# Optimization experiments

Measured on AMD Instinct MI355X. Metric: run time of the kernel, lower is better.

## Reference

```python
import jax, jax.numpy as jnp
import numpy as np

B, T, C = 4, 2048, 2048
H = 16
D = C // H  # head_dim = 128
THETA = 10000.0


def rope_cos_sin(t, d, dtype=jnp.float32):
    inv_freq = 1.0 / (THETA ** (jnp.arange(0, d, 2, dtype=jnp.float32) / d))  # [D/2]
    pos = jnp.arange(t, dtype=jnp.float32)
    freqs = jnp.outer(pos, inv_freq)                 # [T, D/2]
    emb = jnp.concatenate([freqs, freqs], axis=-1)   # [T, D]
    return jnp.cos(emb).astype(dtype), jnp.sin(emb).astype(dtype)


def rotate_half(x):
    x1, x2 = jnp.split(x, 2, axis=-1)
    return jnp.concatenate([-x2, x1], axis=-1)


def setup_inputs() -> dict:
    key = jax.random.key(0)
    k1, k2, k3 = jax.random.split(key, 3)
    x = jax.random.normal(k1, (B, T, C), dtype=jnp.float32)
    Wqkv = jax.random.normal(k2, (C, 3 * C), dtype=jnp.float32) * (1.0 / np.sqrt(C))
    Wout = jax.random.normal(k3, (C, C), dtype=jnp.float32) * (1.0 / np.sqrt(C))
    return {"x": x, "Wqkv": Wqkv, "Wout": Wout}


def reference(x, Wqkv, Wout):
    b, t, c = x.shape
    qkv = jnp.einsum('btc,cd->btd', x, Wqkv)          # [B,T,3C]
    q, k, v = jnp.split(qkv, 3, axis=-1)
    # [B,T,C] -> [B,H,T,D]
    q = q.reshape(b, t, H, D).transpose(0, 2, 1, 3)
    k = k.reshape(b, t, H, D).transpose(0, 2, 1, 3)
    v = v.reshape(b, t, H, D).transpose(0, 2, 1, 3)
    cos, sin = rope_cos_sin(t, D, x.dtype)            # [T,D]
    cos = cos[None, None]                             # [1,1,T,D]
    sin = sin[None, None]
    q = q * cos + rotate_half(q) * sin
    k = k * cos + rotate_half(k) * sin
    scale = 1.0 / np.sqrt(D)
    scores = jnp.einsum('bhqd,bhkd->bhqk', q, k) * scale
    causal = jnp.tril(jnp.ones((t, t), dtype=bool))
    scores = jnp.where(causal[None, None], scores, jnp.finfo(scores.dtype).min)
    attn = jax.nn.softmax(scores, axis=-1)
    y = jnp.einsum('bhqk,bhkd->bhqd', attn, v)        # [B,H,T,D]
    y = y.transpose(0, 2, 1, 3).reshape(b, t, c)      # [B,T,C]
    return jnp.einsum('btc,cd->btd', y, Wout)
```

## Files before the change

### kernel.cpp

```cpp
#include <hip/hip_runtime.h>
#include <hip/hip_bf16.h>
#include <cmath>

#define Bsz   4
#define Tlen  2048
#define Cdim  2048
#define Hn    16
#define Dh    128
#define N_QKV 6144
#define Mrows 8192

typedef __bf16 bf16x8 __attribute__((ext_vector_type(8)));
typedef __bf16 bf16x4 __attribute__((ext_vector_type(4)));
typedef float  f32x4  __attribute__((ext_vector_type(4)));
typedef uint32_t u32x2 __attribute__((ext_vector_type(2)));

__device__ __forceinline__ f32x4 mfma16(bf16x8 a, bf16x8 b, f32x4 c) {
  return __builtin_amdgcn_mfma_f32_16x16x32_bf16(a, b, c, 0, 0, 0);
}

__device__ __forceinline__ void gl16(const void* g, void* l) {
  __builtin_amdgcn_global_load_lds(
      (const __attribute__((address_space(1))) void*)g,
      (__attribute__((address_space(3))) void*)l, 16, 0, 0);
}

__device__ __forceinline__ uint32_t pack_bf16(float lo, float hi) {
  union { __bf16 h; unsigned short u; } a, b;
  a.h = (__bf16)lo; b.h = (__bf16)hi;
  return (uint32_t)a.u | ((uint32_t)b.u << 16);
}

__global__ void rope_table_k(float* __restrict__ cosT, float* __restrict__ sinT) {
  int idx = blockIdx.x * 256 + threadIdx.x;
  int t = idx >> 6, i = idx & 63;
  float invf = __expf(-(float)i * 0.14391156698f);
  float a = (float)t * invf;
  float s, c;
  sincosf(a, &s, &c);
  cosT[idx] = c;
  sinT[idx] = s;
}

__global__ __launch_bounds__(256) void f32_to_bf16_k(
    const float* __restrict__ src, __bf16* __restrict__ dst) {
  size_t i = ((size_t)blockIdx.x * 256 + threadIdx.x) * 8;
  f32x4 a = *(const f32x4*)(src + i);
  f32x4 b = *(const f32x4*)(src + i + 4);
  bf16x8 o;
  o[0] = (__bf16)a[0]; o[1] = (__bf16)a[1]; o[2] = (__bf16)a[2]; o[3] = (__bf16)a[3];
  o[4] = (__bf16)b[0]; o[5] = (__bf16)b[1]; o[6] = (__bf16)b[2]; o[7] = (__bf16)b[3];
  *(bf16x8*)(dst + i) = o;
}

__global__ __launch_bounds__(256) void transpose_to_bf16_k(
    const float* __restrict__ src, __bf16* __restrict__ dst, int K, int N) {
  __shared__ float tile[32][33];
  int n0 = blockIdx.x * 32, k0 = blockIdx.y * 32;
  int tr = threadIdx.x >> 3, tc = (threadIdx.x & 7) * 4;
  f32x4 v = *(const f32x4*)&src[(size_t)(k0 + tr) * N + n0 + tc];
  tile[tr][tc + 0] = v[0]; tile[tr][tc + 1] = v[1];
  tile[tr][tc + 2] = v[2]; tile[tr][tc + 3] = v[3];
  __syncthreads();
  bf16x4 w;
  w[0] = (__bf16)tile[tc + 0][tr];
  w[1] = (__bf16)tile[tc + 1][tr];
  w[2] = (__bf16)tile[tc + 2][tr];
  w[3] = (__bf16)tile[tc + 3][tr];
  *(bf16x4*)&dst[(size_t)(n0 + tr) * K + k0 + tc] = w;
}

__global__ __launch_bounds__(512, 2) void qkv_gemm(
    const __bf16* __restrict__ Xb, const __bf16* __restrict__ Wt,
    __bf16* __restrict__ Qo, __bf16* __restrict__ Ko, __bf16* __restrict__ Vo,
    const float* __restrict__ cosT, const float* __restrict__ sinT)
{
  __shared__ union SM {
    struct { __bf16 A[2][256 * 64]; __bf16 B[2][256 * 64]; } s;
    float C[64][265];
  } sm;

  const int tid = threadIdx.x, lane = tid & 63, wid = tid >> 6;
  const int g = lane >> 4, l16 = lane & 15;
  const int wr = wid >> 2, wc = wid & 3;

  const int bid = blockIdx.x;
  const int xcd = bid & 7, idx = bid >> 3;
  const int stl = idx >> 4, pos = idx & 15;
  const int m0 = (xcd * 4 + (pos >> 2)) * 256;
  const int n0 = (stl * 4 + (pos & 3)) * 256;

  const int srow = tid >> 3;
  const int schk = (tid & 7) ^ (srow & 7);
  const __bf16* gA = Xb + (size_t)(m0 + srow) * Cdim + schk * 8;
  const __bf16* gB = Wt + (size_t)(n0 + srow) * Cdim + schk * 8;
  const int ldst = wid * 512;

  f32x4 acc[8][4] = {};
  const int NT = Cdim / 64;

  #pragma unroll
  for (int r = 0; r < 4; ++r) {
    gl16(gA + (size_t)r * 64 * Cdim, &sm.s.A[0][r * 4096 + ldst]);
    gl16(gB + (size_t)r * 64 * Cdim, &sm.s.B[0][r * 4096 + ldst]);
  }
  #pragma unroll
  for (int r = 0; r < 4; ++r) {
    gl16(gA + 64 + (size_t)r * 64 * Cdim, &sm.s.A[1][r * 4096 + ldst]);
    gl16(gB + 64 + (size_t)r * 64 * Cdim, &sm.s.B[1][r * 4096 + ldst]);
  }

  for (int t = 0; t < NT; ++t) {
    const int p = t & 1;
    if (t < NT - 1) asm volatile("s_waitcnt vmcnt(8)" ::: "memory");
    else            asm volatile("s_waitcnt vmcnt(0)" ::: "memory");
    __builtin_amdgcn_s_barrier();
    __builtin_amdgcn_sched_barrier(0);

    #pragma unroll
    for (int kk = 0; kk < 2; ++kk) {
      bf16x8 a[8], b[4];
      const int ch = (((kk << 2) | g) ^ (l16 & 7)) * 8;
      #pragma unroll
      for (int f = 0; f < 8; ++f)
        a[f] = *(const bf16x8*)&sm.s.A[p][(wr * 128 + f * 16 + l16) * 64 + ch];
      #pragma unroll
      for (int n = 0; n < 4; ++n)
        b[n] = *(const bf16x8*)&sm.s.B[p][(wc * 64 + n * 16 + l16) * 64 + ch];
      #pragma unroll
      for (int f = 0; f < 8; ++f)
        #pragma unroll
        for (int n = 0; n < 4; ++n)
          acc[f][n] = mfma16(a[f], b[n], acc[f][n]);
    }

    __builtin_amdgcn_sched_barrier(0);
    asm volatile("s_waitcnt lgkmcnt(0)" ::: "memory");
    __builtin_amdgcn_s_barrier();

    if (t + 2 < NT) {
      const __bf16* pA = gA + (size_t)(t + 2) * 64;
      const __bf16* pB = gB + (size_t)(t + 2) * 64;
      #pragma unroll
      for (int r = 0; r < 4; ++r) {
        gl16(pA + (size_t)r * 64 * Cdim, &sm.s.A[p][r * 4096 + ldst]);
        gl16(pB + (size_t)r * 64 * Cdim, &sm.s.B[p][r * 4096 + ldst]);
      }
    }
  }

  const int sel = n0 >> 11;
  const int h0  = (n0 & 2047) >> 7;
  const int erow = tid >> 3, q = tid & 7;
  const int dlo = (q & 3) * 16;
  const int clo = (q >> 2) * 128 + dlo;
  const int vcol = tid >> 1, vth = tid & 1;

  #pragma unroll
  for (int rh = 0; rh < 4; ++rh) {
    if (wr == (rh >> 1)) {
      const int fb = (rh & 1) * 4;
      #pragma unroll
      for (int f2 = 0; f2 < 4; ++f2)
        #pragma unroll
        for (int n = 0; n < 4; ++n)
          #pragma unroll
          for (int r = 0; r < 4; ++r)
            sm.C[f2 * 16 + g * 4 + r][wc * 64 + n * 16 + l16] = acc[fb + f2][n][r];
    }
    __syncthreads();
    if (sel == 2) {
      const int hh = h0 + (vcol >> 7), d = vcol & 127;
      const int mb = m0 + rh * 64 + vth * 32;
      const int b_ = mb >> 11, tt = mb & 2047;
      __bf16* outp = Vo + (((size_t)(b_ * Hn + hh)) * Dh + d) * Tlen + tt;
      bf16x8 w[4];
      #pragma unroll
      for (int i = 0; i < 32; ++i)
        w[i >> 3][i & 7] = (__bf16)sm.C[vth * 32 + i][vcol];
      #pragma unroll
      for (int k = 0; k < 4; ++k) *(bf16x8*)&outp[k * 8] = w[k];
    } else {
      __bf16* dst = (sel == 0) ? Qo : Ko;
      const int m = m0 + rh * 64 + erow;
      const int b_ = m >> 11, t = m & 2047;
      __bf16* out = dst + (((size_t)(b_ * Hn + h0 + (q >> 2))) * Tlen + t) * Dh + dlo;
      const float* cb = cosT + t * 64 + dlo;
      const float* sb = sinT + t * 64 + dlo;
      bf16x8 o1[2], o2[2];
      #pragma unroll
      for (int i = 0; i < 16; ++i) {
        float v1 = sm.C[erow][clo + i];
        float v2 = sm.C[erow][clo + i + 64];
        float cs = cb[i], sn = sb[i];
        float r1 = v1 * cs - v2 * sn;
        float r2 = v2 * cs + v1 * sn;
        o1[i >> 3][i & 7] = (__bf16)r1;
        o2[i >> 3][i & 7] = (__bf16)r2;
      }
      *(bf16x8*)&out[0]  = o1[0];
      *(bf16x8*)&out[8]  = o1[1];
      *(bf16x8*)&out[64] = o2[0];
      *(bf16x8*)&out[72] = o2[1];
    }
    __syncthreads();
  }
}

__global__ __launch_bounds__(256, 2) void attn_fwd(
    const __bf16* __restrict__ Qg, const __bf16* __restrict__ Kg,
    const __bf16* __restrict__ Vtg, __bf16* __restrict__ Yg)
{
  __shared__ __bf16 Ks[2][64 * 128];
  __shared__ __bf16 Vt[2][128 * 64];
  __shared__ uint32_t Ps2[4][16 * 34 + 2];

  const int tid = threadIdx.x, lane = tid & 63, wid = tid >> 6;
  const int g = lane >> 4, l16 = lane & 15;
  const int qt = gridDim.x - 1 - blockIdx.x;
  const int q0 = qt * 64;
  const size_t bh = (size_t)blockIdx.z * Hn + blockIdx.y;
  const __bf16* Kbase = Kg + bh * ((size_t)Tlen * Dh);
  const __bf16* Vbase = Vtg + bh * ((size_t)Dh * Tlen);

  const int q_glob = q0 + wid * 16 + l16;

  bf16x8 aq[4];
  {
    const __bf16* qrow = Qg + (bh * Tlen + q_glob) * Dh;
    #pragma unroll
    for (int ks = 0; ks < 4; ++ks)
      aq[ks] = *(const bf16x8*)(qrow + ks * 32 + 8 * g);
  }

  float m_r = -1e30f, l_r = 0.f;
  f32x4 o[8] = {};
  const float k_e = 0.08838834764831845f * 1.4426950408889634f;

  const int NKV = qt + 1;

  const int krow = lane >> 4, kchk = lane & 15;
  const int vrow = lane >> 3, vchk = lane & 7;

#define STAGE_KV(kv0_, buf_)                                                    \
  {                                                                             \
    _Pragma("unroll")                                                           \
    for (int rr = 0; rr < 4; ++rr) {                                            \
      const int row = wid * 16 + rr * 4 + krow;                                 \
      const int sc = kchk ^ (row & 7);                                          \
      gl16(Kbase + (size_t)((kv0_) + row) * Dh + sc * 8,                        \
           &Ks[buf_][(wid * 16 + rr * 4) * 128]);                               \
    }                                                                           \
    _Pragma("unroll")                                                           \
    for (int rr = 0; rr < 4; ++rr) {                                            \
      const int row = wid * 32 + rr * 8 + vrow;                                 \
      const int sc = vchk ^ (row & 7);                                          \
      gl16(Vbase + (size_t)row * Tlen + (kv0_) + sc * 8,                        \
           &Vt[buf_][(wid * 32 + rr * 8) * 64]);                                \
    }                                                                           \
  }

  STAGE_KV(0, 0);

  for (int it = 0; it < NKV; ++it) {
    const int p = it & 1;
    if (it + 1 < NKV) {
      STAGE_KV((it + 1) * 64, (it + 1) & 1);
      asm volatile("s_waitcnt vmcnt(8)" ::: "memory");
    } else {
      asm volatile("s_waitcnt vmcnt(0)" ::: "memory");
    }
    __builtin_amdgcn_s_barrier();
    __builtin_amdgcn_sched_barrier(0);

    f32x4 s[4] = {};
    __builtin_amdgcn_s_setprio(1);
    #pragma unroll
    for (int ks = 0; ks < 4; ++ks) {
      const int ch = ((4 * ks + g) ^ (l16 & 7)) * 8;
      #pragma unroll
      for (int nf = 0; nf < 4; ++nf) {
        bf16x8 bk = *(const bf16x8*)&Ks[p][(nf * 16 + l16) * 128 + ch];
        s[nf] = mfma16(bk, aq[ks], s[nf]);
      }
    }
    __builtin_amdgcn_s_setprio(0);

    if (it == qt) {
      const int kvb = it * 64 + 4 * g;
      #pragma unroll
      for (int nf = 0; nf < 4; ++nf)
        #pragma unroll
        for (int r = 0; r < 4; ++r)
          if (kvb + nf * 16 + r > q_glob) s[nf][r] = -1e30f;
    }

    float mx = s[0][0];
    #pragma unroll
    for (int nf = 0; nf < 4; ++nf)
      #pragma unroll
      for (int r = 0; r < 4; ++r) mx = fmaxf(mx, s[nf][r]);
    mx = fmaxf(mx, __shfl_xor(mx, 16, 64));
    mx = fmaxf(mx, __shfl_xor(mx, 32, 64));

    if (!__all(mx - m_r <= 8.0f)) {
      const float mn = fmaxf(m_r, mx);
      const float al = exp2f((m_r - mn) * k_e);
      m_r = mn;
      l_r *= al;
      #pragma unroll
      for (int n2 = 0; n2 < 8; ++n2)
        #pragma unroll
        for (int r = 0; r < 4; ++r) o[n2][r] *= al;
    }

    const float mk = -m_r * k_e;
    float rs = 0.f;
    #pragma unroll
    for (int nf = 0; nf < 4; ++nf)
      #pragma unroll
      for (int r = 0; r < 4; ++r) {
        const float pv = exp2f(fmaf(s[nf][r], k_e, mk));
        s[nf][r] = pv;
        rs += pv;
      }
    rs += __shfl_xor(rs, 16, 64);
    rs += __shfl_xor(rs, 32, 64);
    l_r += rs;

    #pragma unroll
    for (int nf = 0; nf < 4; ++nf) {
      u32x2 wv;
      wv.x = pack_bf16(s[nf][0], s[nf][1]);
      wv.y = pack_bf16(s[nf][2], s[nf][3]);
      *(u32x2*)&Ps2[wid][l16 * 34 + nf * 8 + 2 * g] = wv;
    }
    asm volatile("s_waitcnt lgkmcnt(0)" ::: "memory");
    __builtin_amdgcn_sched_barrier(0);

    union { u32x2 h[2]; bf16x8 v; } pb0, pb1;
    pb0.h[0] = *(const u32x2*)&Ps2[wid][l16 * 34 + 4 * g];
    pb0.h[1] = *(const u32x2*)&Ps2[wid][l16 * 34 + 4 * g + 2];
    pb1.h[0] = *(const u32x2*)&Ps2[wid][l16 * 34 + 16 + 4 * g];
    pb1.h[1] = *(const u32x2*)&Ps2[wid][l16 * 34 + 16 + 4 * g + 2];

    const int c0 = (g ^ (l16 & 7)) * 8;
    const int c1 = ((4 + g) ^ (l16 & 7)) * 8;
    __builtin_amdgcn_s_setprio(1);
    #pragma unroll
    for (int n2 = 0; n2 < 8; ++n2) {
      bf16x8 vb0 = *(const bf16x8*)&Vt[p][(n2 * 16 + l16) * 64 + c0];
      bf16x8 vb1 = *(const bf16x8*)&Vt[p][(n2 * 16 + l16) * 64 + c1];
      o[n2] = mfma16(vb0, pb0.v, o[n2]);
      o[n2] = mfma16(vb1, pb1.v, o[n2]);
    }
    __builtin_amdgcn_s_setprio(0);

    asm volatile("s_waitcnt lgkmcnt(0)" ::: "memory");
    __builtin_amdgcn_sched_barrier(0);
    __builtin_amdgcn_s_barrier();
  }
#undef STAGE_KV

  const float inv = 1.0f / l_r;
  __bf16* yrow = Yg + ((size_t)(blockIdx.z * Tlen + q0 + wid * 16 + l16)) * Cdim
               + blockIdx.y * Dh;
  #pragma unroll
  for (int n2 = 0; n2 < 8; ++n2) {
    bf16x4 w;
    #pragma unroll
    for (int r = 0; r < 4; ++r) w[r] = (__bf16)(o[n2][r] * inv);
    *(bf16x4*)&yrow[n2 * 16 + 4 * g] = w;
  }
}

__global__ __launch_bounds__(512, 2) void out_gemm(
    const __bf16* __restrict__ Yb, const __bf16* __restrict__ Wt,
    float* __restrict__ O)
{
  __shared__ struct { __bf16 A[2][256 * 64]; __bf16 B[2][256 * 64]; } sm;

  const int tid = threadIdx.x, lane = tid & 63, wid = tid >> 6;
  const int g = lane >> 4, l16 = lane & 15;
  const int wr = wid >> 2, wc = wid & 3;

  const int bid = blockIdx.x;
  const int xcd = bid & 7, idx = bid >> 3;
  const int stl = idx >> 4, pos = idx & 15;
  const int m0 = (xcd * 4 + (pos >> 2)) * 256;
  const int n0 = (stl * 4 + (pos & 3)) * 256;

  const int srow = tid >> 3;
  const int schk = (tid & 7) ^ (srow & 7);
  const __bf16* gA = Yb + (size_t)(m0 + srow) * Cdim + schk * 8;
  const __bf16* gB = Wt + (size_t)(n0 + srow) * Cdim + schk * 8;
  const int ldst = wid * 512;

  f32x4 acc[8][4] = {};
  const int NT = Cdim / 64;

  #pragma unroll
  for (int r = 0; r < 4; ++r) {
    gl16(gA + (size_t)r * 64 * Cdim, &sm.A[0][r * 4096 + ldst]);
    gl16(gB + (size_t)r * 64 * Cdim, &sm.B[0][r * 4096 + ldst]);
  }
  #pragma unroll
  for (int r = 0; r < 4; ++r) {
    gl16(gA + 64 + (size_t)r * 64 * Cdim, &sm.A[1][r * 4096 + ldst]);
    gl16(gB + 64 + (size_t)r * 64 * Cdim, &sm.B[1][r * 4096 + ldst]);
  }

  for (int t = 0; t < NT; ++t) {
    const int p = t & 1;
    if (t < NT - 1) asm volatile("s_waitcnt vmcnt(8)" ::: "memory");
    else            asm volatile("s_waitcnt vmcnt(0)" ::: "memory");
    __builtin_amdgcn_s_barrier();
    __builtin_amdgcn_sched_barrier(0);

    #pragma unroll
    for (int kk = 0; kk < 2; ++kk) {
      bf16x8 a[8], b[4];
      const int ch = (((kk << 2) | g) ^ (l16 & 7)) * 8;
      #pragma unroll
      for (int f = 0; f < 8; ++f)
        a[f] = *(const bf16x8*)&sm.A[p][(wr * 128 + f * 16 + l16) * 64 + ch];
      #pragma unroll
      for (int n = 0; n < 4; ++n)
        b[n] = *(const bf16x8*)&sm.B[p][(wc * 64 + n * 16 + l16) * 64 + ch];
      #pragma unroll
      for (int f = 0; f < 8; ++f)
        #pragma unroll
        for (int n = 0; n < 4; ++n)
          acc[f][n] = mfma16(a[f], b[n], acc[f][n]);
    }

    __builtin_amdgcn_sched_barrier(0);
    asm volatile("s_waitcnt lgkmcnt(0)" ::: "memory");
    __builtin_amdgcn_s_barrier();

    if (t + 2 < NT) {
      const __bf16* pA = gA + (size_t)(t + 2) * 64;
      const __bf16* pB = gB + (size_t)(t + 2) * 64;
      #pragma unroll
      for (int r = 0; r < 4; ++r) {
        gl16(pA + (size_t)r * 64 * Cdim, &sm.A[p][r * 4096 + ldst]);
        gl16(pB + (size_t)r * 64 * Cdim, &sm.B[p][r * 4096 + ldst]);
      }
    }
  }

  #pragma unroll
  for (int f = 0; f < 8; ++f)
    #pragma unroll
    for (int n = 0; n < 4; ++n)
      #pragma unroll
      for (int r = 0; r < 4; ++r)
        O[(size_t)(m0 + wr * 128 + f * 16 + g * 4 + r) * Cdim
          + (n0 + wc * 64 + n * 16 + l16)] = acc[f][n][r];
}

extern "C" void kernel_launch(void* const* d_in, const int* in_sizes, int n_in,
                              void* d_out, int out_size, void* d_ws, size_t ws_size,
                              hipStream_t stream) {
  const float* x    = (const float*)d_in[0];
  const float* Wqkv = (const float*)d_in[1];
  const float* Wout = (const float*)d_in[2];
  float* out = (float*)d_out;

  float*  cosT   = (float*)d_ws;
  float*  sinT   = cosT + Tlen * 64;
  __bf16* Xb     = (__bf16*)(sinT + Tlen * 64);
  __bf16* Wqkv_t = Xb + (size_t)Mrows * Cdim;
  __bf16* Wout_t = Wqkv_t + (size_t)N_QKV * Cdim;
  __bf16* Qb     = Wout_t + (size_t)Cdim * Cdim;
  __bf16* Kb     = Qb + (size_t)Bsz * Hn * Tlen * Dh;
  __bf16* Vb     = Kb + (size_t)Bsz * Hn * Tlen * Dh;
  __bf16* Yb     = Xb;

  rope_table_k<<<dim3(512), dim3(256), 0, stream>>>(cosT, sinT);
  f32_to_bf16_k<<<dim3(Mrows * Cdim / (256 * 8)), dim3(256), 0, stream>>>(x, Xb);
  transpose_to_bf16_k<<<dim3(N_QKV / 32, Cdim / 32), dim3(256), 0, stream>>>(
      Wqkv, Wqkv_t, Cdim, N_QKV);
  transpose_to_bf16_k<<<dim3(Cdim / 32, Cdim / 32), dim3(256), 0, stream>>>(
      Wout, Wout_t, Cdim, Cdim);
  qkv_gemm<<<dim3(768), dim3(512), 0, stream>>>(
      Xb, Wqkv_t, Qb, Kb, Vb, cosT, sinT);
  attn_fwd<<<dim3(Tlen / 64, Hn, Bsz), dim3(256), 0, stream>>>(Qb, Kb, Vb, Yb);
  out_gemm<<<dim3(256), dim3(512), 0, stream>>>(Yb, Wout_t, out);
}
```

Measured before the change: 665.4 us.

## Halve GEMM K-tile to 32 and raise occupancy to four blocks per CU

```diff
diff --git a/kernel.cpp b/kernel.cpp
--- a/kernel.cpp
+++ b/kernel.cpp
@@ -70,19 +70,20 @@
   *(bf16x4*)&dst[(size_t)(n0 + tr) * K + k0 + tc] = w;
 }
 
-__global__ __launch_bounds__(512, 2) void qkv_gemm(
+__global__ __launch_bounds__(512, 4) void qkv_gemm(
     const __bf16* __restrict__ Xb, const __bf16* __restrict__ Wt,
     __bf16* __restrict__ Qo, __bf16* __restrict__ Ko, __bf16* __restrict__ Vo,
     const float* __restrict__ cosT, const float* __restrict__ sinT)
 {
   __shared__ union SM {
-    struct { __bf16 A[2][256 * 64]; __bf16 B[2][256 * 64]; } s;
+    struct { __bf16 A[2][256 * 32]; __bf16 B[2][256 * 32]; } s;
     float C[64][265];
   } sm;
 
   const int tid = threadIdx.x, lane = tid & 63, wid = tid >> 6;
   const int g = lane >> 4, l16 = lane & 15;
   const int wr = wid >> 2, wc = wid & 3;
+  const int sr0 = lane >> 2;
 
   const int bid = blockIdx.x;
   const int xcd = bid & 7, idx = bid >> 3;
@@ -90,43 +91,38 @@
   const int m0 = (xcd * 4 + (pos >> 2)) * 256;
   const int n0 = (stl * 4 + (pos & 3)) * 256;
 
-  const int srow = tid >> 3;
-  const int schk = (tid & 7) ^ (srow & 7);
-  const __bf16* gA = Xb + (size_t)(m0 + srow) * Cdim + schk * 8;
-  const __bf16* gB = Wt + (size_t)(n0 + srow) * Cdim + schk * 8;
-  const int ldst = wid * 512;
-
   f32x4 acc[8][4] = {};
-  const int NT = Cdim / 64;
-
-  #pragma unroll
-  for (int r = 0; r < 4; ++r) {
-    gl16(gA + (size_t)r * 64 * Cdim, &sm.s.A[0][r * 4096 + ldst]);
-    gl16(gB + (size_t)r * 64 * Cdim, &sm.s.B[0][r * 4096 + ldst]);
-  }
-  #pragma unroll
-  for (int r = 0; r < 4; ++r) {
-    gl16(gA + 64 + (size_t)r * 64 * Cdim, &sm.s.A[1][r * 4096 + ldst]);
-    gl16(gB + 64 + (size_t)r * 64 * Cdim, &sm.s.B[1][r * 4096 + ldst]);
-  }
+  const int NT = Cdim / 32;
+
+#define QSTAGE(buf_, t_) {                                                    \
+    _Pragma("unroll") for (int j = 0; j < 2; ++j) {                           \
+      const int rr = wid * 32 + j * 16 + sr0;                                 \
+      const int sc = (lane & 3) ^ ((rr >> 1) & 3);                            \
+      gl16(Xb + (size_t)(m0 + rr) * Cdim + (t_) * 32 + sc * 8,                \
+           &sm.s.A[buf_][(wid * 32 + j * 16) * 32]);                          \
+      gl16(Wt + (size_t)(n0 + rr) * Cdim + (t_) * 32 + sc * 8,                \
+           &sm.s.B[buf_][(wid * 32 + j * 16) * 32]);                          \
+    } }
+
+  QSTAGE(0, 0)
+  QSTAGE(1, 1)
 
   for (int t = 0; t < NT; ++t) {
     const int p = t & 1;
-    if (t < NT - 1) asm volatile("s_waitcnt vmcnt(8)" ::: "memory");
+    if (t < NT - 1) asm volatile("s_waitcnt vmcnt(4)" ::: "memory");
     else            asm volatile("s_waitcnt vmcnt(0)" ::: "memory");
     __builtin_amdgcn_s_barrier();
     __builtin_amdgcn_sched_barrier(0);
 
-    #pragma unroll
-    for (int kk = 0; kk < 2; ++kk) {
+    {
       bf16x8 a[8], b[4];
-      const int ch = (((kk << 2) | g) ^ (l16 & 7)) * 8;
+      const int ch = (g ^ ((l16 >> 1) & 3)) * 8;
       #pragma unroll
       for (int f = 0; f < 8; ++f)
-        a[f] = *(const bf16x8*)&sm.s.A[p][(wr * 128 + f * 16 + l16) * 64 + ch];
+        a[f] = *(const bf16x8*)&sm.s.A[p][(wr * 128 + f * 16 + l16) * 32 + ch];
       #pragma unroll
       for (int n = 0; n < 4; ++n)
-        b[n] = *(const bf16x8*)&sm.s.B[p][(wc * 64 + n * 16 + l16) * 64 + ch];
+        b[n] = *(const bf16x8*)&sm.s.B[p][(wc * 64 + n * 16 + l16) * 32 + ch];
       #pragma unroll
       for (int f = 0; f < 8; ++f)
         #pragma unroll
@@ -138,16 +134,9 @@
     asm volatile("s_waitcnt lgkmcnt(0)" ::: "memory");
     __builtin_amdgcn_s_barrier();
 
-    if (t + 2 < NT) {
-      const __bf16* pA = gA + (size_t)(t + 2) * 64;
-      const __bf16* pB = gB + (size_t)(t + 2) * 64;
-      #pragma unroll
-      for (int r = 0; r < 4; ++r) {
-        gl16(pA + (size_t)r * 64 * Cdim, &sm.s.A[p][r * 4096 + ldst]);
-        gl16(pB + (size_t)r * 64 * Cdim, &sm.s.B[p][r * 4096 + ldst]);
-      }
-    }
-  }
+    if (t + 2 < NT) QSTAGE(p, t + 2)
+  }
+#undef QSTAGE
 
   const int sel = n0 >> 11;
   const int h0  = (n0 & 2047) >> 7;
@@ -374,15 +363,16 @@
   }
 }
 
-__global__ __launch_bounds__(512, 2) void out_gemm(
+__global__ __launch_bounds__(512, 4) void out_gemm(
     const __bf16* __restrict__ Yb, const __bf16* __restrict__ Wt,
     float* __restrict__ O)
 {
-  __shared__ struct { __bf16 A[2][256 * 64]; __bf16 B[2][256 * 64]; } sm;
+  __shared__ struct { __bf16 A[2][256 * 32]; __bf16 B[2][256 * 32]; } sm;
 
   const int tid = threadIdx.x, lane = tid & 63, wid = tid >> 6;
   const int g = lane >> 4, l16 = lane & 15;
   const int wr = wid >> 2, wc = wid & 3;
+  const int sr0 = lane >> 2;
 
   const int bid = blockIdx.x;
   const int xcd = bid & 7, idx = bid >> 3;
@@ -390,43 +380,38 @@
   const int m0 = (xcd * 4 + (pos >> 2)) * 256;
   const int n0 = (stl * 4 + (pos & 3)) * 256;
 
-  const int srow = tid >> 3;
-  const int schk = (tid & 7) ^ (srow & 7);
-  const __bf16* gA = Yb + (size_t)(m0 + srow) * Cdim + schk * 8;
-  const __bf16* gB = Wt + (size_t)(n0 + srow) * Cdim + schk * 8;
-  const int ldst = wid * 512;
-
   f32x4 acc[8][4] = {};
-  const int NT = Cdim / 64;
-
-  #pragma unroll
-  for (int r = 0; r < 4; ++r) {
-    gl16(gA + (size_t)r * 64 * Cdim, &sm.A[0][r * 4096 + ldst]);
-    gl16(gB + (size_t)r * 64 * Cdim, &sm.B[0][r * 4096 + ldst]);
-  }
-  #pragma unroll
-  for (int r = 0; r < 4; ++r) {
-    gl16(gA + 64 + (size_t)r * 64 * Cdim, &sm.A[1][r * 4096 + ldst]);
-    gl16(gB + 64 + (size_t)r * 64 * Cdim, &sm.B[1][r * 4096 + ldst]);
-  }
+  const int NT = Cdim / 32;
+
+#define OSTAGE(buf_, t_) {                                                    \
+    _Pragma("unroll") for (int j = 0; j < 2; ++j) {                           \
+      const int rr = wid * 32 + j * 16 + sr0;                                 \
+      const int sc = (lane & 3) ^ ((rr >> 1) & 3);                            \
+      gl16(Yb + (size_t)(m0 + rr) * Cdim + (t_) * 32 + sc * 8,                \
+           &sm.A[buf_][(wid * 32 + j * 16) * 32]);                            \
+      gl16(Wt + (size_t)(n0 + rr) * Cdim + (t_) * 32 + sc * 8,                \
+           &sm.B[buf_][(wid * 32 + j * 16) * 32]);                            \
+    } }
+
+  OSTAGE(0, 0)
+  OSTAGE(1, 1)
 
   for (int t = 0; t < NT; ++t) {
     const int p = t & 1;
-    if (t < NT - 1) asm volatile("s_waitcnt vmcnt(8)" ::: "memory");
+    if (t < NT - 1) asm volatile("s_waitcnt vmcnt(4)" ::: "memory");
     else            asm volatile("s_waitcnt vmcnt(0)" ::: "memory");
     __builtin_amdgcn_s_barrier();
     __builtin_amdgcn_sched_barrier(0);
 
-    #pragma unroll
-    for (int kk = 0; kk < 2; ++kk) {
+    {
       bf16x8 a[8], b[4];
-      const int ch = (((kk << 2) | g) ^ (l16 & 7)) * 8;
+      const int ch = (g ^ ((l16 >> 1) & 3)) * 8;
       #pragma unroll
       for (int f = 0; f < 8; ++f)
-        a[f] = *(const bf16x8*)&sm.A[p][(wr * 128 + f * 16 + l16) * 64 + ch];
+        a[f] = *(const bf16x8*)&sm.A[p][(wr * 128 + f * 16 + l16) * 32 + ch];
       #pragma unroll
       for (int n = 0; n < 4; ++n)
-        b[n] = *(const bf16x8*)&sm.B[p][(wc * 64 + n * 16 + l16) * 64 + ch];
+        b[n] = *(const bf16x8*)&sm.B[p][(wc * 64 + n * 16 + l16) * 32 + ch];
       #pragma unroll
       for (int f = 0; f < 8; ++f)
         #pragma unroll
@@ -438,16 +423,9 @@
     asm volatile("s_waitcnt lgkmcnt(0)" ::: "memory");
     __builtin_amdgcn_s_barrier();
 
-    if (t + 2 < NT) {
-      const __bf16* pA = gA + (size_t)(t + 2) * 64;
-      const __bf16* pB = gB + (size_t)(t + 2) * 64;
-      #pragma unroll
-      for (int r = 0; r < 4; ++r) {
-        gl16(pA + (size_t)r * 64 * Cdim, &sm.A[p][r * 4096 + ldst]);
-        gl16(pB + (size_t)r * 64 * Cdim, &sm.B[p][r * 4096 + ldst]);
-      }
-    }
-  }
+    if (t + 2 < NT) OSTAGE(p, t + 2)
+  }
+#undef OSTAGE
 
   #pragma unroll
   for (int f = 0; f < 8; ++f)
```

After: 1.921 ms. 189% more time.
